# Optimization experiments

Measured on AMD Instinct MI355X. Metric: run time of the kernel, lower is better.

## Reference

```python
import jax, jax.numpy as jnp
import numpy as np


def setup_inputs() -> dict:
    key = jax.random.key(0)
    ks = jax.random.split(key, 6)
    B, Cx, Cf, Ch, H, W = 4, 512, 512, 256, 64, 64
    return {
        "query_features": jax.random.normal(ks[0], (B, Cx, H, W), dtype=jnp.float32),
        "reference_features": jax.random.normal(ks[1], (B, Cf, H, W), dtype=jnp.float32),
        "Wq": jax.random.normal(ks[2], (Ch, Cx), dtype=jnp.float32) * (1.0 / np.sqrt(Cx)),
        "bq": jax.random.normal(ks[3], (Ch,), dtype=jnp.float32) * 0.02,
        "Wk": jax.random.normal(ks[4], (Ch, Cf), dtype=jnp.float32) * (1.0 / np.sqrt(Cf)),
        "bk": jax.random.normal(ks[5], (Ch,), dtype=jnp.float32) * 0.02,
    }


def reference(query_features, reference_features, Wq, bq, Wk, bk):
    # 1x1 convs == per-pixel linear projections over channels
    Q = jnp.einsum('bchw,oc->bohw', query_features, Wq) + bq[None, :, None, None]
    K = jnp.einsum('bchw,oc->bohw', reference_features, Wk) + bk[None, :, None, None]
    B, Cf, H2, W2 = reference_features.shape
    H1, W1 = Q.shape[2], Q.shape[3]
    V = reference_features.reshape(B, Cf, H2 * W2)            # b c p
    # unscaled QK^T over hidden channels: [b, h1, w1, h2*w2]
    scores = jnp.einsum('bcij,bckl->bijkl', Q, K).reshape(B, H1, W1, H2 * W2)
    attn = jax.nn.softmax(scores, axis=-1)
    out = jnp.einsum('bijp,bcp->bcij', attn, V)               # [b, Cf, h1, w1]
    return out
```

## Files before the change

### kernel.cpp

```cpp
#include <hip/hip_runtime.h>
#include <hip/hip_bf16.h>
#include <hip/hip_fp16.h>

typedef _Float16 half8 __attribute__((ext_vector_type(8)));
typedef _Float16 half4v __attribute__((ext_vector_type(4)));
typedef float f4 __attribute__((ext_vector_type(4)));
typedef float f16v __attribute__((ext_vector_type(16)));
typedef short short8 __attribute__((ext_vector_type(8)));
typedef unsigned short us8 __attribute__((ext_vector_type(8)));
typedef int i4 __attribute__((ext_vector_type(4)));

#define P_SZ 4096
#define CH 256
#define CIN 512
#define CV 512
#define KVB 32
#define L2E 1.4426950408889634f

__device__ __forceinline__ unsigned short f2bf(float f) {
  unsigned u = __float_as_uint(f);
  unsigned r = u + 0x7fffu + ((u >> 16) & 1u);
  return (unsigned short)(r >> 16);
}
__device__ __forceinline__ float bf2f(unsigned short h) {
  return __uint_as_float(((unsigned)h) << 16);
}

__device__ __forceinline__ void gload16(const void* g, void* l) {
  __builtin_amdgcn_global_load_lds(
      (const __attribute__((address_space(1))) unsigned int*)g,
      (__attribute__((address_space(3))) unsigned int*)l, 16, 0, 0);
}

__global__ __launch_bounds__(256) void wconv_kernel(
    const float* __restrict__ Wq, const float* __restrict__ Wk,
    short* __restrict__ Wh, short* __restrict__ Wl) {
  const int i = blockIdx.x * 256 + threadIdx.x;
  const int which = i >> 17;
  const int j = i & 131071;
  const float w = which ? Wk[j] : Wq[j] * L2E;
  const unsigned short h = f2bf(w);
  Wh[i] = (short)h;
  Wl[i] = (short)f2bf(w - bf2f(h));
}

__global__ __launch_bounds__(256) void vconv_kernel(const float* __restrict__ in,
                                                    _Float16* __restrict__ outv) {
  __shared__ _Float16 T[512][34];
  const int b = blockIdx.x >> 7;
  const int tile = blockIdx.x & 127;
  const int tid = threadIdx.x;
  const float* src = in + (size_t)b * CIN * P_SZ + tile * 32;
  const int c0 = tid >> 3, j4 = tid & 7;
  #pragma unroll
  for (int pass = 0; pass < 16; ++pass) {
    const int c = pass * 32 + c0;
    const f4 x = *(const f4*)(src + (size_t)c * P_SZ + j4 * 4);
    half4v h;
    h[0] = (_Float16)x[0]; h[1] = (_Float16)x[1];
    h[2] = (_Float16)x[2]; h[3] = (_Float16)x[3];
    *(half4v*)&T[c][j4 * 4] = h;
  }
  __syncthreads();
  _Float16* dst = outv + (size_t)b * 2097152 + (size_t)tile * 16384;
  #pragma unroll
  for (int i = 0; i < 8; ++i) {
    const int kh = i >> 1;
    const int ch = ((i & 1) << 8) + tid;
    *(half8*)(dst + kh * 4096 + ch * 8) = *(const half8*)&T[ch][kh * 8];
  }
}

__global__ __launch_bounds__(512) void proj_kernel(
    const float* __restrict__ Xq, const float* __restrict__ bq,
    const float* __restrict__ Xk, const float* __restrict__ bk,
    const short* __restrict__ Wh, const short* __restrict__ Wl,
    _Float16* __restrict__ Qout, _Float16* __restrict__ Kout) {
  const int which = blockIdx.z;
  const float* __restrict__ X = which ? Xk : Xq;
  const float* __restrict__ bias = which ? bk : bq;
  _Float16* __restrict__ out = which ? Kout : Qout;
  const float bscale = which ? 1.f : L2E;

  const int b = blockIdx.y;
  const int p0 = blockIdx.x * 64;
  const int tid = threadIdx.x;
  const int w = tid >> 6, l = tid & 63;
  const int wp = w >> 2, wo = w & 3;
  const int lr = l & 15, lg = l >> 4;

  const float* __restrict__ Xb = X + (size_t)b * CIN * P_SZ;
  const short* __restrict__ Whb = Wh + (size_t)which * 131072;
  const short* __restrict__ Wlb = Wl + (size_t)which * 131072;

  f4 acc[2][4];
  #pragma unroll
  for (int m = 0; m < 2; ++m)
    #pragma unroll
    for (int n = 0; n < 4; ++n) acc[m][n] = (f4){0.f, 0.f, 0.f, 0.f};

  const int prow0 = p0 + wp * 32 + lr;

  #pragma unroll 1
  for (int kc = 0; kc < CIN; kc += 32) {
    short8 ah[2], al[2];
    #pragma unroll
    for (int m = 0; m < 2; ++m) {
      const float* xp = Xb + (size_t)(kc + lg * 8) * P_SZ + (prow0 + m * 16);
      #pragma unroll
      for (int i = 0; i < 8; ++i) {
        float xv = xp[(size_t)i * P_SZ];
        unsigned short h = f2bf(xv);
        ah[m][i] = (short)h;
        al[m][i] = (short)f2bf(xv - bf2f(h));
      }
    }
    short8 bh[4], bl[4];
    #pragma unroll
    for (int n = 0; n < 4; ++n) {
      const size_t wi = (size_t)(wo * 64 + n * 16 + lr) * CIN + kc + lg * 8;
      bh[n] = *(const short8*)(Whb + wi);
      bl[n] = *(const short8*)(Wlb + wi);
    }
    #pragma unroll
    for (int m = 0; m < 2; ++m)
      #pragma unroll
      for (int n = 0; n < 4; ++n) {
        acc[m][n] = __builtin_amdgcn_mfma_f32_16x16x32_bf16(ah[m], bh[n], acc[m][n], 0, 0, 0);
        acc[m][n] = __builtin_amdgcn_mfma_f32_16x16x32_bf16(ah[m], bl[n], acc[m][n], 0, 0, 0);
        acc[m][n] = __builtin_amdgcn_mfma_f32_16x16x32_bf16(al[m], bh[n], acc[m][n], 0, 0, 0);
      }
  }

  #pragma unroll
  for (int n = 0; n < 4; ++n) {
    const int o = wo * 64 + n * 16 + lr;
    const float bv = bias[o] * bscale;
    #pragma unroll
    for (int m = 0; m < 2; ++m) {
      #pragma unroll
      for (int j = 0; j < 4; ++j) {
        const int p = p0 + wp * 32 + m * 16 + lg * 4 + j;
        const _Float16 val = (_Float16)(acc[m][n][j] + bv);
        if (which == 0) {
          out[((size_t)b * P_SZ + p) * CH + o] = val;
        } else {
          const int kk = p & 31;
          const int kswz = (kk & 19) | ((kk & 4) << 1) | ((kk & 8) >> 1);
          out[(size_t)b * 1048576 + (size_t)(p >> 5) * 8192
              + (size_t)(o >> 3) * 256 + kswz * 8 + (o & 7)] = val;
        }
      }
    }
  }
}

template <int NSEG, bool DIRECT>
__global__ __launch_bounds__(512, 2) void attn_kernel(
    const _Float16* __restrict__ Qg, const _Float16* __restrict__ Kt,
    const _Float16* __restrict__ Vt, unsigned short* __restrict__ Opart,
    float* __restrict__ Mp, float* __restrict__ Lp, float* __restrict__ Og) {
  __shared__ char K_l[3][16384];
  __shared__ char V_l[3][32768];

  constexpr int nt = (P_SZ / NSEG) / KVB;
  int b, qt, seg;
  if (NSEG == 2) {
    const int g = blockIdx.x & 7;
    b = g >> 1; seg = g & 1; qt = blockIdx.x >> 3;
  } else {
    b = blockIdx.x & 3; seg = 0; qt = blockIdx.x >> 2;
  }

  const int tid = threadIdx.x;
  const int w = tid >> 6, l = tid & 63;
  const int hi = l >> 5, l31 = l & 31;
  const int wq = w >> 1, half = w & 1;

  const char* Kb = (const char*)Kt + (size_t)b * 2097152 + (size_t)seg * nt * 16384;
  const char* Vb = (const char*)Vt + (size_t)b * 4194304 + (size_t)seg * nt * 32768;

#define STAGE(BUF, T) do { \
    const char* ksrc = Kb + (size_t)(T) * 16384; \
    const char* vsrc = Vb + (size_t)(T) * 32768; \
    gload16(ksrc + tid * 16,         &K_l[BUF][w * 1024]); \
    gload16(ksrc + 8192 + tid * 16,  &K_l[BUF][8192 + w * 1024]); \
    gload16(vsrc + tid * 16,         &V_l[BUF][w * 1024]); \
    gload16(vsrc + 8192 + tid * 16,  &V_l[BUF][8192 + w * 1024]); \
    gload16(vsrc + 16384 + tid * 16, &V_l[BUF][16384 + w * 1024]); \
    gload16(vsrc + 24576 + tid * 16, &V_l[BUF][24576 + w * 1024]); \
  } while (0)

  half8 qf[16];
  {
    const char* qrow = (const char*)Qg +
        ((size_t)b * P_SZ + qt * 128 + wq * 32 + l31) * 512;
    #pragma unroll
    for (int m = 0; m < 16; ++m) qf[m] = *(const half8*)(qrow + m * 32 + hi * 16);
  }

  f16v acc[8];
  #pragma unroll
  for (int n = 0; n < 8; ++n)
    acc[n] = (f16v){0,0,0,0, 0,0,0,0, 0,0,0,0, 0,0,0,0};

  float m_run = -1e30f, lsum = 0.f;
  const int kread = hi * 512 + l31 * 16;
  const int vread = hi * 8192 + half * 4096 + l31 * 16;

  STAGE(0, 0); STAGE(1, 1);
  asm volatile("s_waitcnt vmcnt(6)" ::: "memory");
  asm volatile("s_barrier" ::: "memory");
  __builtin_amdgcn_sched_barrier(0);

  int bufc = 0;
  #pragma unroll 1
  for (int t = 0; t < nt; ++t) {
    const char* kb = &K_l[bufc][0] + kread;
    f16v s0_ = (f16v){0,0,0,0, 0,0,0,0, 0,0,0,0, 0,0,0,0};
    f16v s1_ = (f16v){0,0,0,0, 0,0,0,0, 0,0,0,0, 0,0,0,0};
    __builtin_amdgcn_s_setprio(1);
    #pragma unroll
    for (int m = 0; m < 8; ++m) {
      half8 kf0 = *(const half8*)(kb + m * 1024);
      half8 kf1 = *(const half8*)(kb + (m + 8) * 1024);
      s0_ = __builtin_amdgcn_mfma_f32_32x32x16_f16(kf0, qf[m], s0_, 0, 0, 0);
      s1_ = __builtin_amdgcn_mfma_f32_32x32x16_f16(kf1, qf[m + 8], s1_, 0, 0, 0);
    }
    __builtin_amdgcn_s_setprio(0);
    const f16v s = s0_ + s1_;

    float x0 = fmaxf(s[0], s[8]),  x1 = fmaxf(s[1], s[9]);
    float x2 = fmaxf(s[2], s[10]), x3 = fmaxf(s[3], s[11]);
    float x4 = fmaxf(s[4], s[12]), x5 = fmaxf(s[5], s[13]);
    float x6 = fmaxf(s[6], s[14]), x7 = fmaxf(s[7], s[15]);
    x0 = fmaxf(x0, x4); x1 = fmaxf(x1, x5); x2 = fmaxf(x2, x6); x3 = fmaxf(x3, x7);
    float pm = fmaxf(fmaxf(x0, x1), fmaxf(x2, x3));
    pm = fmaxf(pm, __shfl_xor(pm, 32));
    if (__any(pm > m_run + 12.f)) {
      const float mnew = fmaxf(m_run, pm);
      const float al = __builtin_amdgcn_exp2f(m_run - mnew);
      const int alb = __float_as_int(al);
      #pragma unroll
      for (int r = 0; r < 16; ++r) {
        const int cr = (r & 3) + 8 * (r >> 2);
        const float ar = __int_as_float(
            __builtin_amdgcn_ds_bpermute(cr * 4 + hi * 16, alb));
        #pragma unroll
        for (int n = 0; n < 8; ++n) acc[n][r] *= ar;
      }
      lsum *= al;
      m_run = mnew;
    }
    float p[16], psum;
    #pragma unroll
    for (int r = 0; r < 16; ++r) p[r] = __builtin_amdgcn_exp2f(s[r] - m_run);
    {
      float a0 = (p[0] + p[1]) + (p[2] + p[3]);
      float a1 = (p[4] + p[5]) + (p[6] + p[7]);
      float a2 = (p[8] + p[9]) + (p[10] + p[11]);
      float a3 = (p[12] + p[13]) + (p[14] + p[15]);
      psum = (a0 + a1) + (a2 + a3);
      psum += __shfl_xor(psum, 32);
    }
    lsum += psum;

    i4 w0v, w1v;
    w0v[0] = __builtin_bit_cast(int, __builtin_amdgcn_cvt_pkrtz(p[0], p[1]));
    w0v[1] = __builtin_bit_cast(int, __builtin_amdgcn_cvt_pkrtz(p[2], p[3]));
    w0v[2] = __builtin_bit_cast(int, __builtin_amdgcn_cvt_pkrtz(p[4], p[5]));
    w0v[3] = __builtin_bit_cast(int, __builtin_amdgcn_cvt_pkrtz(p[6], p[7]));
    w1v[0] = __builtin_bit_cast(int, __builtin_amdgcn_cvt_pkrtz(p[8], p[9]));
    w1v[1] = __builtin_bit_cast(int, __builtin_amdgcn_cvt_pkrtz(p[10], p[11]));
    w1v[2] = __builtin_bit_cast(int, __builtin_amdgcn_cvt_pkrtz(p[12], p[13]));
    w1v[3] = __builtin_bit_cast(int, __builtin_amdgcn_cvt_pkrtz(p[14], p[15]));
    const half8 pa0 = __builtin_bit_cast(half8, w0v);
    const half8 pa1 = __builtin_bit_cast(half8, w1v);

    const int bufs = bufc == 0 ? 2 : bufc - 1;
    if (t + 2 < nt) STAGE(bufs, t + 2);

    const char* vb = &V_l[bufc][0] + vread;
    __builtin_amdgcn_s_setprio(1);
    #pragma unroll
    for (int n = 0; n < 8; ++n) {
      half8 v0 = *(const half8*)(vb + n * 512);
      acc[n] = __builtin_amdgcn_mfma_f32_32x32x16_f16(pa0, v0, acc[n], 0, 0, 0);
      half8 v1 = *(const half8*)(vb + 16384 + n * 512);
      acc[n] = __builtin_amdgcn_mfma_f32_32x32x16_f16(pa1, v1, acc[n], 0, 0, 0);
    }
    __builtin_amdgcn_s_setprio(0);

    if (t + 2 < nt) { asm volatile("s_waitcnt vmcnt(6)" ::: "memory"); }
    else            { asm volatile("s_waitcnt vmcnt(0)" ::: "memory"); }
    asm volatile("s_barrier" ::: "memory");
    __builtin_amdgcn_sched_barrier(0);
    bufc = bufc == 2 ? 0 : bufc + 1;
  }
#undef STAGE

  const int qg0 = qt * 128 + wq * 32;
  if (!DIRECT) {
    unsigned short* Ob = Opart +
        (((size_t)seg * 4 + b) * P_SZ + qg0) * 512 + half * 256 + l31;
    #pragma unroll
    for (int n = 0; n < 8; ++n) {
      #pragma unroll
      for (int r = 0; r < 16; ++r) {
        const int q = (r & 3) + 8 * (r >> 2) + 4 * hi;
        Ob[(size_t)q * 512 + n * 32] = f2bf(acc[n][r]);
      }
    }
    if (half == 0 && l < 32) {
      const size_t mi = ((size_t)seg * 4 + b) * P_SZ + qg0 + l31;
      Mp[mi] = m_run; Lp[mi] = lsum;
    }
  } else {
    float linv[16];
    const int lb = __float_as_int(lsum);
    #pragma unroll
    for (int r = 0; r < 16; ++r) {
      const int cr = (r & 3) + 8 * (r >> 2);
      const float lq = __int_as_float(__builtin_amdgcn_ds_bpermute(cr * 4 + hi * 16, lb));
      linv[r] = 1.f / lq;
    }
    #pragma unroll
    for (int n = 0; n < 8; ++n) {
      #pragma unroll
      for (int r = 0; r < 16; ++r) {
        const int q = (r & 3) + 8 * (r >> 2) + 4 * hi;
        Og[((size_t)b * CV + half * 256 + n * 32 + l31) * P_SZ + qg0 + q] =
            acc[n][r] * linv[r];
      }
    }
  }
}

template <int NSEG>
__global__ __launch_bounds__(256) void combine_kernel(
    const unsigned short* __restrict__ Opart, const float* __restrict__ Mp,
    const float* __restrict__ Lp, float* __restrict__ Og) {
  __shared__ float T[64][65];
  const int bx = blockIdx.x;
  const int ct = bx & 7, qt = (bx >> 3) & 63, b = bx >> 9;
  const int tid = threadIdx.x;
  {
    const int qi = tid >> 2, cj = tid & 3;
    const int q = qt * 64 + qi;
    const size_t mibase = (size_t)b * P_SZ + q;
    float M = -1e30f;
    #pragma unroll
    for (int s = 0; s < NSEG; ++s) M = fmaxf(M, Mp[(size_t)s * 4 * P_SZ + mibase]);
    float L = 0.f;
    float o[16];
    #pragma unroll
    for (int e = 0; e < 16; ++e) o[e] = 0.f;
    #pragma unroll
    for (int s = 0; s < NSEG; ++s) {
      const float wgt = __builtin_amdgcn_exp2f(Mp[(size_t)s * 4 * P_SZ + mibase] - M);
      L += wgt * Lp[(size_t)s * 4 * P_SZ + mibase];
      const unsigned short* src = Opart +
          (((size_t)s * 4 + b) * P_SZ + q) * 512 + ct * 64 + cj * 16;
      const us8 ua = ((const us8*)src)[0];
      const us8 ub = ((const us8*)src)[1];
      #pragma unroll
      for (int e = 0; e < 8; ++e) {
        o[e]     += wgt * bf2f(ua[e]);
        o[8 + e] += wgt * bf2f(ub[e]);
      }
    }
    const float inv = 1.f / L;
    #pragma unroll
    for (int e = 0; e < 16; ++e) T[qi][cj * 16 + e] = o[e] * inv;
  }
  __syncthreads();
  const int ci = tid >> 2, qj = tid & 3;
  #pragma unroll
  for (int i = 0; i < 4; ++i) {
    f4 v;
    #pragma unroll
    for (int e = 0; e < 4; ++e) v[e] = T[qj * 16 + i * 4 + e][ci];
    *(f4*)&Og[((size_t)b * CV + ct * 64 + ci) * P_SZ + qt * 64 + qj * 16 + i * 4] = v;
  }
}

extern "C" void kernel_launch(void* const* d_in, const int* in_sizes, int n_in,
                              void* d_out, int out_size, void* d_ws, size_t ws_size,
                              hipStream_t stream) {
  const float* x  = (const float*)d_in[0];
  const float* f  = (const float*)d_in[1];
  const float* Wq = (const float*)d_in[2];
  const float* bq = (const float*)d_in[3];
  const float* Wk = (const float*)d_in[4];
  const float* bk = (const float*)d_in[5];
  float* out = (float*)d_out;

  char* ws = (char*)d_ws;
  _Float16* Qf = (_Float16*)ws;
  _Float16* Kf = (_Float16*)(ws + ((size_t)8 << 20));
  _Float16* Vf = (_Float16*)(ws + ((size_t)16 << 20));
  float* Mp    = (float*)(ws + ((size_t)32 << 20));
  float* Lp    = (float*)(ws + ((size_t)32 << 20) + (256 << 10));
  short* Wh    = (short*)(ws + ((size_t)32 << 20) + (512 << 10));
  short* Wl    = (short*)(ws + ((size_t)33 << 20));
  unsigned short* Opart = (unsigned short*)(ws + ((size_t)34 << 20));

  wconv_kernel<<<dim3(1024), dim3(256), 0, stream>>>(Wq, Wk, Wh, Wl);
  vconv_kernel<<<dim3(512), dim3(256), 0, stream>>>(f, Vf);
  proj_kernel<<<dim3(64, 4, 2), dim3(512), 0, stream>>>(x, bq, f, bk, Wh, Wl, Qf, Kf);

  const size_t need2 = ((size_t)34 << 20) + ((size_t)32 << 20);
  const size_t need1 = ((size_t)34 << 20) + ((size_t)16 << 20);
  if (ws_size >= need2) {
    attn_kernel<2, false><<<dim3(256), dim3(512), 0, stream>>>(Qf, Kf, Vf, Opart, Mp, Lp, nullptr);
    combine_kernel<2><<<dim3(2048), dim3(256), 0, stream>>>(Opart, Mp, Lp, out);
  } else if (ws_size >= need1) {
    attn_kernel<1, false><<<dim3(128), dim3(512), 0, stream>>>(Qf, Kf, Vf, Opart, Mp, Lp, nullptr);
    combine_kernel<1><<<dim3(2048), dim3(256), 0, stream>>>(Opart, Mp, Lp, out);
  } else {
    attn_kernel<1, true><<<dim3(128), dim3(512), 0, stream>>>(Qf, Kf, Vf, nullptr, nullptr, nullptr, out);
  }
}
```

Before: 257.7 us.

## Software-pipeline PV MFMA of previous tile with softmax of current tile

```diff
diff --git a/kernel.cpp b/kernel.cpp
--- a/kernel.cpp
+++ b/kernel.cpp
@@ -180,11 +180,13 @@
   const char* Kb = (const char*)Kt + (size_t)b * 2097152 + (size_t)seg * nt * 16384;
   const char* Vb = (const char*)Vt + (size_t)b * 4194304 + (size_t)seg * nt * 32768;
 
-#define STAGE(BUF, T) do { \
+#define STAGE_K(BUF, T) do { \
     const char* ksrc = Kb + (size_t)(T) * 16384; \
-    const char* vsrc = Vb + (size_t)(T) * 32768; \
     gload16(ksrc + tid * 16,         &K_l[BUF][w * 1024]); \
     gload16(ksrc + 8192 + tid * 16,  &K_l[BUF][8192 + w * 1024]); \
+  } while (0)
+#define STAGE_V(BUF, T) do { \
+    const char* vsrc = Vb + (size_t)(T) * 32768; \
     gload16(vsrc + tid * 16,         &V_l[BUF][w * 1024]); \
     gload16(vsrc + 8192 + tid * 16,  &V_l[BUF][8192 + w * 1024]); \
     gload16(vsrc + 16384 + tid * 16, &V_l[BUF][16384 + w * 1024]); \
@@ -208,7 +210,9 @@
   const int kread = hi * 512 + l31 * 16;
   const int vread = hi * 8192 + half * 4096 + l31 * 16;
 
-  STAGE(0, 0); STAGE(1, 1);
+  half8 pa0p, pa1p;
+
+  STAGE_K(0, 0); STAGE_K(1, 1); STAGE_V(0, 0);
   asm volatile("s_waitcnt vmcnt(6)" ::: "memory");
   asm volatile("s_barrier" ::: "memory");
   __builtin_amdgcn_sched_barrier(0);
@@ -216,19 +220,18 @@
   int bufc = 0;
   #pragma unroll 1
   for (int t = 0; t < nt; ++t) {
+    const int bprev = bufc == 0 ? 2 : bufc - 1;
+    const int bnext = bufc == 2 ? 0 : bufc + 1;
+
     const char* kb = &K_l[bufc][0] + kread;
-    f16v s0_ = (f16v){0,0,0,0, 0,0,0,0, 0,0,0,0, 0,0,0,0};
-    f16v s1_ = (f16v){0,0,0,0, 0,0,0,0, 0,0,0,0, 0,0,0,0};
+    f16v s = (f16v){0,0,0,0, 0,0,0,0, 0,0,0,0, 0,0,0,0};
     __builtin_amdgcn_s_setprio(1);
     #pragma unroll
-    for (int m = 0; m < 8; ++m) {
-      half8 kf0 = *(const half8*)(kb + m * 1024);
-      half8 kf1 = *(const half8*)(kb + (m + 8) * 1024);
-      s0_ = __builtin_amdgcn_mfma_f32_32x32x16_f16(kf0, qf[m], s0_, 0, 0, 0);
-      s1_ = __builtin_amdgcn_mfma_f32_32x32x16_f16(kf1, qf[m + 8], s1_, 0, 0, 0);
+    for (int m = 0; m < 16; ++m) {
+      half8 kf = *(const half8*)(kb + m * 1024);
+      s = __builtin_amdgcn_mfma_f32_32x32x16_f16(kf, qf[m], s, 0, 0, 0);
     }
     __builtin_amdgcn_s_setprio(0);
-    const f16v s = s0_ + s1_;
 
     float x0 = fmaxf(s[0], s[8]),  x1 = fmaxf(s[1], s[9]);
     float x2 = fmaxf(s[2], s[10]), x3 = fmaxf(s[3], s[11]);
@@ -237,24 +240,26 @@
     x0 = fmaxf(x0, x4); x1 = fmaxf(x1, x5); x2 = fmaxf(x2, x6); x3 = fmaxf(x3, x7);
     float pm = fmaxf(fmaxf(x0, x1), fmaxf(x2, x3));
     pm = fmaxf(pm, __shfl_xor(pm, 32));
-    if (__any(pm > m_run + 12.f)) {
-      const float mnew = fmaxf(m_run, pm);
-      const float al = __builtin_amdgcn_exp2f(m_run - mnew);
-      const int alb = __float_as_int(al);
-      #pragma unroll
-      for (int r = 0; r < 16; ++r) {
-        const int cr = (r & 3) + 8 * (r >> 2);
-        const float ar = __int_as_float(
-            __builtin_amdgcn_ds_bpermute(cr * 4 + hi * 16, alb));
-        #pragma unroll
-        for (int n = 0; n < 8; ++n) acc[n][r] *= ar;
-      }
-      lsum *= al;
-      m_run = mnew;
-    }
-    float p[16], psum;
-    #pragma unroll
-    for (int r = 0; r < 16; ++r) p[r] = __builtin_amdgcn_exp2f(s[r] - m_run);
+    const bool trig = __any(pm > m_run + 12.f);
+    const float mnew = trig ? fmaxf(m_run, pm) : m_run;
+
+    if (t > 0) {
+      const char* vb = &V_l[bprev][0] + vread;
+      __builtin_amdgcn_s_setprio(1);
+      #pragma unroll
+      for (int n = 0; n < 8; ++n) {
+        half8 v0 = *(const half8*)(vb + n * 512);
+        acc[n] = __builtin_amdgcn_mfma_f32_32x32x16_f16(pa0p, v0, acc[n], 0, 0, 0);
+        half8 v1 = *(const half8*)(vb + 16384 + n * 512);
+        acc[n] = __builtin_amdgcn_mfma_f32_32x32x16_f16(pa1p, v1, acc[n], 0, 0, 0);
+      }
+      __builtin_amdgcn_s_setprio(0);
+    }
+
+    float p[16];
+    #pragma unroll
+    for (int r = 0; r < 16; ++r) p[r] = __builtin_amdgcn_exp2f(s[r] - mnew);
+    float psum;
     {
       float a0 = (p[0] + p[1]) + (p[2] + p[3]);
       float a1 = (p[4] + p[5]) + (p[6] + p[7]);
@@ -263,6 +268,21 @@
       psum = (a0 + a1) + (a2 + a3);
       psum += __shfl_xor(psum, 32);
     }
+
+    if (trig) {
+      const float al = __builtin_amdgcn_exp2f(m_run - mnew);
+      const int alb = __float_as_int(al);
+      #pragma unroll
+      for (int r = 0; r < 16; ++r) {
+        const int cr = (r & 3) + 8 * (r >> 2);
+        const float ar = __int_as_float(
+            __builtin_amdgcn_ds_bpermute(cr * 4 + hi * 16, alb));
+        #pragma unroll
+        for (int n = 0; n < 8; ++n) acc[n][r] *= ar;
+      }
+      lsum *= al;
+    }
+    m_run = mnew;
     lsum += psum;
 
     i4 w0v, w1v;
@@ -274,30 +294,33 @@
     w1v[1] = __builtin_bit_cast(int, __builtin_amdgcn_cvt_pkrtz(p[10], p[11]));
     w1v[2] = __builtin_bit_cast(int, __builtin_amdgcn_cvt_pkrtz(p[12], p[13]));
     w1v[3] = __builtin_bit_cast(int, __builtin_amdgcn_cvt_pkrtz(p[14], p[15]));
-    const half8 pa0 = __builtin_bit_cast(half8, w0v);
-    const half8 pa1 = __builtin_bit_cast(half8, w1v);
-
-    const int bufs = bufc == 0 ? 2 : bufc - 1;
-    if (t + 2 < nt) STAGE(bufs, t + 2);
-
-    const char* vb = &V_l[bufc][0] + vread;
-    __builtin_amdgcn_s_setprio(1);
+    pa0p = __builtin_bit_cast(half8, w0v);
+    pa1p = __builtin_bit_cast(half8, w1v);
+
+    if (t + 2 < nt) STAGE_K(bprev, t + 2);
+    if (t + 1 < nt) STAGE_V(bnext, t + 1);
+
+    if (t + 2 < nt)      { asm volatile("s_waitcnt vmcnt(6)" ::: "memory"); }
+    else if (t + 1 < nt) { asm volatile("s_waitcnt vmcnt(4)" ::: "memory"); }
+    else                 { asm volatile("s_waitcnt vmcnt(0)" ::: "memory"); }
+    asm volatile("s_barrier" ::: "memory");
+    __builtin_amdgcn_sched_barrier(0);
+    bufc = bnext;
+  }
+
+  {
+    const int bprev = bufc == 0 ? 2 : bufc - 1;
+    const char* vb = &V_l[bprev][0] + vread;
     #pragma unroll
     for (int n = 0; n < 8; ++n) {
       half8 v0 = *(const half8*)(vb + n * 512);
-      acc[n] = __builtin_amdgcn_mfma_f32_32x32x16_f16(pa0, v0, acc[n], 0, 0, 0);
+      acc[n] = __builtin_amdgcn_mfma_f32_32x32x16_f16(pa0p, v0, acc[n], 0, 0, 0);
       half8 v1 = *(const half8*)(vb + 16384 + n * 512);
-      acc[n] = __builtin_amdgcn_mfma_f32_32x32x16_f16(pa1, v1, acc[n], 0, 0, 0);
-    }
-    __builtin_amdgcn_s_setprio(0);
-
-    if (t + 2 < nt) { asm volatile("s_waitcnt vmcnt(6)" ::: "memory"); }
-    else            { asm volatile("s_waitcnt vmcnt(0)" ::: "memory"); }
-    asm volatile("s_barrier" ::: "memory");
-    __builtin_amdgcn_sched_barrier(0);
-    bufc = bufc == 2 ? 0 : bufc + 1;
-  }
-#undef STAGE
+      acc[n] = __builtin_amdgcn_mfma_f32_32x32x16_f16(pa1p, v1, acc[n], 0, 0, 0);
+    }
+  }
+#undef STAGE_K
+#undef STAGE_V
 
   const int qg0 = qt * 128 + wq * 32;
   if (!DIRECT) {
```

New measurement: 259.3 us. About the same (+0.6%).

## Stage projection input through LDS transpose and use single QK accumulator chain

Applied to the files above, without the earlier changes.

```diff
diff --git a/kernel.cpp b/kernel.cpp
--- a/kernel.cpp
+++ b/kernel.cpp
@@ -76,6 +76,7 @@
     const float* __restrict__ Xk, const float* __restrict__ bk,
     const short* __restrict__ Wh, const short* __restrict__ Wl,
     _Float16* __restrict__ Qout, _Float16* __restrict__ Kout) {
+  __shared__ float Xs[64][65];
   const int which = blockIdx.z;
   const float* __restrict__ X = which ? Xk : Xq;
   const float* __restrict__ bias = which ? bk : bq;
@@ -99,37 +100,54 @@
     #pragma unroll
     for (int n = 0; n < 4; ++n) acc[m][n] = (f4){0.f, 0.f, 0.f, 0.f};
 
-  const int prow0 = p0 + wp * 32 + lr;
+  const int crow = tid >> 4;
+  const int pq4 = (tid & 15) * 4;
 
   #pragma unroll 1
-  for (int kc = 0; kc < CIN; kc += 32) {
-    short8 ah[2], al[2];
-    #pragma unroll
-    for (int m = 0; m < 2; ++m) {
-      const float* xp = Xb + (size_t)(kc + lg * 8) * P_SZ + (prow0 + m * 16);
-      #pragma unroll
-      for (int i = 0; i < 8; ++i) {
-        float xv = xp[(size_t)i * P_SZ];
-        unsigned short h = f2bf(xv);
-        ah[m][i] = (short)h;
-        al[m][i] = (short)f2bf(xv - bf2f(h));
-      }
-    }
-    short8 bh[4], bl[4];
-    #pragma unroll
-    for (int n = 0; n < 4; ++n) {
-      const size_t wi = (size_t)(wo * 64 + n * 16 + lr) * CIN + kc + lg * 8;
-      bh[n] = *(const short8*)(Whb + wi);
-      bl[n] = *(const short8*)(Wlb + wi);
-    }
-    #pragma unroll
-    for (int m = 0; m < 2; ++m)
+  for (int kc64 = 0; kc64 < CIN; kc64 += 64) {
+    __syncthreads();
+    #pragma unroll
+    for (int h2 = 0; h2 < 2; ++h2) {
+      const int c = crow + h2 * 32;
+      const f4 x = *(const f4*)(Xb + (size_t)(kc64 + c) * P_SZ + p0 + pq4);
+      Xs[pq4 + 0][c] = x[0];
+      Xs[pq4 + 1][c] = x[1];
+      Xs[pq4 + 2][c] = x[2];
+      Xs[pq4 + 3][c] = x[3];
+    }
+    __syncthreads();
+
+    #pragma unroll
+    for (int s = 0; s < 2; ++s) {
+      const int kc = kc64 + s * 32;
+      short8 ah[2], al[2];
+      #pragma unroll
+      for (int m = 0; m < 2; ++m) {
+        const int pl = wp * 32 + m * 16 + lr;
+        #pragma unroll
+        for (int i = 0; i < 8; ++i) {
+          float xv = Xs[pl][s * 32 + lg * 8 + i];
+          unsigned short h = f2bf(xv);
+          ah[m][i] = (short)h;
+          al[m][i] = (short)f2bf(xv - bf2f(h));
+        }
+      }
+      short8 bh[4], bl[4];
       #pragma unroll
       for (int n = 0; n < 4; ++n) {
-        acc[m][n] = __builtin_amdgcn_mfma_f32_16x16x32_bf16(ah[m], bh[n], acc[m][n], 0, 0, 0);
-        acc[m][n] = __builtin_amdgcn_mfma_f32_16x16x32_bf16(ah[m], bl[n], acc[m][n], 0, 0, 0);
-        acc[m][n] = __builtin_amdgcn_mfma_f32_16x16x32_bf16(al[m], bh[n], acc[m][n], 0, 0, 0);
-      }
+        const size_t wi = (size_t)(wo * 64 + n * 16 + lr) * CIN + kc + lg * 8;
+        bh[n] = *(const short8*)(Whb + wi);
+        bl[n] = *(const short8*)(Wlb + wi);
+      }
+      #pragma unroll
+      for (int m = 0; m < 2; ++m)
+        #pragma unroll
+        for (int n = 0; n < 4; ++n) {
+          acc[m][n] = __builtin_amdgcn_mfma_f32_16x16x32_bf16(ah[m], bh[n], acc[m][n], 0, 0, 0);
+          acc[m][n] = __builtin_amdgcn_mfma_f32_16x16x32_bf16(ah[m], bl[n], acc[m][n], 0, 0, 0);
+          acc[m][n] = __builtin_amdgcn_mfma_f32_16x16x32_bf16(al[m], bh[n], acc[m][n], 0, 0, 0);
+        }
+    }
   }
 
   #pragma unroll
@@ -211,24 +229,19 @@
   STAGE(0, 0); STAGE(1, 1);
   asm volatile("s_waitcnt vmcnt(6)" ::: "memory");
   asm volatile("s_barrier" ::: "memory");
-  __builtin_amdgcn_sched_barrier(0);
 
   int bufc = 0;
   #pragma unroll 1
   for (int t = 0; t < nt; ++t) {
     const char* kb = &K_l[bufc][0] + kread;
-    f16v s0_ = (f16v){0,0,0,0, 0,0,0,0, 0,0,0,0, 0,0,0,0};
-    f16v s1_ = (f16v){0,0,0,0, 0,0,0,0, 0,0,0,0, 0,0,0,0};
+    f16v s = (f16v){0,0,0,0, 0,0,0,0, 0,0,0,0, 0,0,0,0};
     __builtin_amdgcn_s_setprio(1);
     #pragma unroll
-    for (int m = 0; m < 8; ++m) {
-      half8 kf0 = *(const half8*)(kb + m * 1024);
-      half8 kf1 = *(const half8*)(kb + (m + 8) * 1024);
-      s0_ = __builtin_amdgcn_mfma_f32_32x32x16_f16(kf0, qf[m], s0_, 0, 0, 0);
-      s1_ = __builtin_amdgcn_mfma_f32_32x32x16_f16(kf1, qf[m + 8], s1_, 0, 0, 0);
+    for (int m = 0; m < 16; ++m) {
+      half8 kf = *(const half8*)(kb + m * 1024);
+      s = __builtin_amdgcn_mfma_f32_32x32x16_f16(kf, qf[m], s, 0, 0, 0);
     }
     __builtin_amdgcn_s_setprio(0);
-    const f16v s = s0_ + s1_;
 
     float x0 = fmaxf(s[0], s[8]),  x1 = fmaxf(s[1], s[9]);
     float x2 = fmaxf(s[2], s[10]), x3 = fmaxf(s[3], s[11]);
@@ -294,7 +307,6 @@
     if (t + 2 < nt) { asm volatile("s_waitcnt vmcnt(6)" ::: "memory"); }
     else            { asm volatile("s_waitcnt vmcnt(0)" ::: "memory"); }
     asm volatile("s_barrier" ::: "memory");
-    __builtin_amdgcn_sched_barrier(0);
     bufc = bufc == 2 ? 0 : bufc + 1;
   }
 #undef STAGE
```

After: 262.4 us. Within noise of the previous version (+1.8%).
